# Optimization experiments

Hardware: AMD Instinct MI355X
Metric: run time of the kernel (lower is better)

## Reference

```python
import jax, jax.numpy as jnp
import numpy as np

NOT_EPSILON = 1.0
B, S, D = 1, 512, 256


def swishmax(x, axis):
    xexp = x * jnp.exp(x - jnp.max(x, axis=axis, keepdims=True))
    return xexp / (jnp.sum(jnp.abs(xexp), axis=axis, keepdims=True) + NOT_EPSILON)


def setup_inputs() -> dict:
    key = jax.random.key(0)
    ks = jax.random.split(key, 13)
    scale = 1.0 / np.sqrt(D)
    mk = lambda k: jax.random.uniform(k, (D, D), jnp.float32, -scale, scale)
    mb = lambda k: jax.random.uniform(k, (D,), jnp.float32, -scale, scale)
    return {
        "query_tokens": jax.random.normal(ks[0], (B, S, D), jnp.float32),
        "key_tokens": jax.random.normal(ks[1], (B, S, D), jnp.float32),
        "value_tokens": jax.random.normal(ks[2], (B, S, D), jnp.float32),
        "Wk": mk(ks[3]), "bk": mb(ks[4]),
        "Wq": mk(ks[5]), "bq": mb(ks[6]),
        "Wva": mk(ks[7]), "bva": mb(ks[8]),
        "Wl": mk(ks[9]), "bl": mb(ks[10]),
        "Wvo": mk(ks[11]), "bvo": mb(ks[12]),
    }


def reference(query_tokens, key_tokens, value_tokens,
              Wk, bk, Wq, bq, Wva, bva, Wl, bl, Wvo, bvo):
    # residual linear transforms of tokens
    k = key_tokens + key_tokens @ Wk + bk        # [B,S,D]
    q = query_tokens + query_tokens @ Wq + bq    # [B,S,D]
    # batchify: key -> [B,Sk,1,D], query -> [B,1,Sq,D]; outer-product scores
    attention_raw = k[:, :, None, :] * q[:, None, :, :]          # [B,Sk,Sq,D]
    attention_logits = attention_raw + attention_raw @ Wl + bl   # DxD linear on raw scores
    attention_scale = swishmax(attention_logits, axis=-2)        # normalize over query axis (dim -shape_dims)
    v = value_tokens + value_tokens @ Wva + bva  # [B,S,D]
    values_scaled = v[:, :, None, :] * attention_scale           # [B,Sk,Sq,D]
    value_sum = values_scaled.sum(axis=-3)                       # reduce key axis -> [B,Sq,D]
    value_out = value_sum + value_sum @ Wvo + bvo
    return value_out
```

## Files before the change

### kernel.cpp

```cpp
#include <hip/hip_runtime.h>
#include <math.h>

#define S_LEN 512
#define D_DIM 256
#define SLICE (S_LEN * D_DIM)

typedef _Float16 half8  __attribute__((ext_vector_type(8)));
typedef _Float16 half4v __attribute__((ext_vector_type(4)));
typedef float   floatx4 __attribute__((ext_vector_type(4)));

__global__ __launch_bounds__(256) void prep_wl(const float* __restrict__ Wl,
                                               _Float16* __restrict__ WlhT)
{
    const int d = blockIdx.x, e = threadIdx.x;
    float v = Wl[e * D_DIM + d] + (e == d ? 1.0f : 0.0f);
    WlhT[d * D_DIM + e] = (_Float16)v;
}

__global__ __launch_bounds__(256) void cvt_fp16(const float* __restrict__ kf,
                                                const float* __restrict__ qf,
                                                _Float16* __restrict__ kh,
                                                _Float16* __restrict__ qh)
{
    const int i = (blockIdx.x * 256 + threadIdx.x) * 4;
    float4 a = *(const float4*)(kf + i);
    float4 b = *(const float4*)(qf + i);
    half4v ah = { (_Float16)a.x, (_Float16)a.y, (_Float16)a.z, (_Float16)a.w };
    half4v bh = { (_Float16)b.x, (_Float16)b.y, (_Float16)b.z, (_Float16)b.w };
    *(half4v*)(kh + i) = ah;
    *(half4v*)(qh + i) = bh;
}

__global__ __launch_bounds__(256) void linres3(
    const float* __restrict__ xk, const float* __restrict__ Wk,
    const float* __restrict__ bk, float* __restrict__ yk,
    const float* __restrict__ xq, const float* __restrict__ Wq,
    const float* __restrict__ bq, float* __restrict__ yq,
    const float* __restrict__ xv, const float* __restrict__ Wv,
    const float* __restrict__ bv, float* __restrict__ yv)
{
    __shared__ float xs[4][D_DIM];
    const int r0 = blockIdx.x * 4;
    const int sel = blockIdx.y;
    const float* x = sel == 0 ? xk : (sel == 1 ? xq : xv);
    const float* W = sel == 0 ? Wk : (sel == 1 ? Wq : Wv);
    const float* b = sel == 0 ? bk : (sel == 1 ? bq : bv);
    float*       y = sel == 0 ? yk : (sel == 1 ? yq : yv);

    const int tid = threadIdx.x;
    #pragma unroll
    for (int t = 0; t < 4; ++t) xs[t][tid] = x[(r0 + t) * D_DIM + tid];
    __syncthreads();
    const float bv_ = b[tid];
    float acc[4];
    #pragma unroll
    for (int i = 0; i < 4; ++i) acc[i] = xs[i][tid] + bv_;
    #pragma unroll 4
    for (int e = 0; e < D_DIM; ++e) {
        const float w = W[e * D_DIM + tid];
        #pragma unroll
        for (int i = 0; i < 4; ++i) acc[i] += xs[i][e] * w;
    }
    #pragma unroll
    for (int i = 0; i < 4; ++i) y[(r0 + i) * D_DIM + tid] = acc[i];
}

__global__ __launch_bounds__(256) void linres_sum(
    const float* __restrict__ po, const float* __restrict__ W,
    const float* __restrict__ b, float* __restrict__ y)
{
    __shared__ float xs[4][D_DIM];
    const int tid = threadIdx.x;
    const int r0  = blockIdx.x * 4;
    #pragma unroll
    for (int t = 0; t < 4; ++t) {
        float s = 0.f;
        #pragma unroll
        for (int c = 0; c < 16; ++c)
            s += po[(size_t)c * SLICE + (r0 + t) * D_DIM + tid];
        xs[t][tid] = s;
    }
    __syncthreads();
    const float bv_ = b[tid];
    float acc[4];
    #pragma unroll
    for (int i = 0; i < 4; ++i) acc[i] = xs[i][tid] + bv_;
    #pragma unroll 4
    for (int e = 0; e < D_DIM; ++e) {
        const float w = W[e * D_DIM + tid];
        #pragma unroll
        for (int i = 0; i < 4; ++i) acc[i] += xs[i][e] * w;
    }
    #pragma unroll
    for (int i = 0; i < 4; ++i) y[(r0 + i) * D_DIM + tid] = acc[i];
}

__device__ __forceinline__ void stage_q(const _Float16* __restrict__ qh,
                                        _Float16* __restrict__ Afrag,
                                        int sq0, int tid)
{
    const int i   = tid & 63;
    const int qtr = tid >> 6;
    const int mt = i >> 4, l16 = i & 15;
    const half8* src = (const half8*)(qh + (size_t)(sq0 + i) * D_DIM + qtr * 64);
    #pragma unroll
    for (int u = 0; u < 8; ++u) {
        const int eb   = qtr * 8 + u;
        const int kk   = eb >> 2, quad = eb & 3;
        const int addr16 = (mt * 8 + kk) * 64 + quad * 16 + l16;
        *(half8*)(Afrag + addr16 * 8) = src[u];
    }
}

__device__ __forceinline__ void stage_q32(const _Float16* __restrict__ qh,
                                          _Float16* __restrict__ Afrag,
                                          int sq0, int tid)
{
    const int i   = tid & 31;
    const int oct = tid >> 5;
    const int mt = i >> 4, l16 = i & 15;
    const half8* src = (const half8*)(qh + (size_t)(sq0 + i) * D_DIM);
    #pragma unroll
    for (int u = 0; u < 4; ++u) {
        const int eb   = oct * 4 + u;
        const int kk   = eb >> 2, quad = eb & 3;
        const int addr16 = (mt * 8 + kk) * 64 + quad * 16 + l16;
        *(half8*)(Afrag + addr16 * 8) = src[eb];
    }
}

__global__ __launch_bounds__(256, 2) void stats_mfma(
    const _Float16* __restrict__ qh, const _Float16* __restrict__ kh,
    const _Float16* __restrict__ WlhT, const float* __restrict__ bl,
    float* __restrict__ pm, float* __restrict__ ps)
{
    __shared__ _Float16 Afrag[32 * 64 * 8];

    const int tid  = threadIdx.x;
    const int lane = tid & 63, wave = tid >> 6;
    const int quad = lane >> 4, l16 = lane & 15;
    const int sqt  = blockIdx.x, sq0 = sqt * 64;
    const int dw   = blockIdx.y * 128 + wave * 32;
    const int sk0  = blockIdx.z * 16;

    stage_q(qh, Afrag, sq0, tid);

    half8 wl[2][8];
    #pragma unroll
    for (int nt = 0; nt < 2; ++nt) {
        const int d = dw + nt * 16 + l16;
        #pragma unroll
        for (int kk = 0; kk < 8; ++kk)
            wl[nt][kk] = *(const half8*)(WlhT + (size_t)d * D_DIM + kk * 32 + quad * 8);
    }
    float bl_r[2];
    #pragma unroll
    for (int nt = 0; nt < 2; ++nt)
        bl_r[nt] = bl[dw + nt * 16 + l16];

    __syncthreads();

    #pragma unroll 1
    for (int s = 0; s < 16; ++s) {
        const int sk = sk0 + s;
        floatx4 acc[4][2];
        #pragma unroll
        for (int mt = 0; mt < 4; ++mt)
            #pragma unroll
            for (int nt = 0; nt < 2; ++nt)
                acc[mt][nt] = (floatx4){0.f, 0.f, 0.f, 0.f};

        #pragma unroll
        for (int kk = 0; kk < 8; ++kk) {
            const half8 k8 = *(const half8*)(kh + (size_t)sk * D_DIM + kk * 32 + quad * 8);
            half8 af[4], bf[2];
            #pragma unroll
            for (int mt = 0; mt < 4; ++mt)
                af[mt] = *(const half8*)(Afrag + ((mt * 8 + kk) * 64 + lane) * 8);
            #pragma unroll
            for (int nt = 0; nt < 2; ++nt)
                bf[nt] = wl[nt][kk] * k8;
            #pragma unroll
            for (int mt = 0; mt < 4; ++mt)
                #pragma unroll
                for (int nt = 0; nt < 2; ++nt)
                    acc[mt][nt] = __builtin_amdgcn_mfma_f32_16x16x32_f16(
                        af[mt], bf[nt], acc[mt][nt], 0, 0, 0);
        }

        #pragma unroll
        for (int nt = 0; nt < 2; ++nt) {
            float Lv[4][4];
            float tmax = -1e30f;
            #pragma unroll
            for (int mt = 0; mt < 4; ++mt)
                #pragma unroll
                for (int r = 0; r < 4; ++r) {
                    const float L = acc[mt][nt][r] + bl_r[nt];
                    Lv[mt][r] = L;
                    tmax = fmaxf(tmax, L);
                }
            float tsum = 0.f;
            #pragma unroll
            for (int mt = 0; mt < 4; ++mt)
                #pragma unroll
                for (int r = 0; r < 4; ++r)
                    tsum += fabsf(Lv[mt][r]) * __expf(Lv[mt][r] - tmax);

            float m = tmax, ss = tsum;
            #pragma unroll
            for (int mask = 16; mask <= 32; mask <<= 1) {
                float m2 = __shfl_xor(m, mask, 64);
                float s2 = __shfl_xor(ss, mask, 64);
                float M  = fmaxf(m, m2);
                ss = ss * __expf(m - M) + s2 * __expf(m2 - M);
                m = M;
            }
            if (quad == 0) {
                const int d = dw + nt * 16 + l16;
                pm[((size_t)sqt * S_LEN + sk) * D_DIM + d] = m;
                ps[((size_t)sqt * S_LEN + sk) * D_DIM + d] = ss;
            }
        }
    }
}

__global__ __launch_bounds__(256) void reduce_ms(
    const float* __restrict__ pm, const float* __restrict__ ps,
    float* __restrict__ mbuf, float* __restrict__ sbuf)
{
    const int idx = blockIdx.x * 256 + threadIdx.x;
    float m = pm[idx], ss = ps[idx];
    #pragma unroll
    for (int t = 1; t < 8; ++t) {
        const float m2 = pm[t * SLICE + idx];
        const float s2 = ps[t * SLICE + idx];
        const float M  = fmaxf(m, m2);
        ss = ss * __expf(m - M) + s2 * __expf(m2 - M);
        m = M;
    }
    mbuf[idx] = m;
    sbuf[idx] = ss;
}

__global__ __launch_bounds__(256, 2) void accum_mfma(
    const _Float16* __restrict__ qh, const _Float16* __restrict__ kh,
    const _Float16* __restrict__ WlhT, const float* __restrict__ bl,
    const float* __restrict__ mbuf, const float* __restrict__ sbuf,
    const float* __restrict__ vbuf, float* __restrict__ po)
{
    __shared__ _Float16 Afrag[16 * 64 * 8];

    const int tid  = threadIdx.x;
    const int lane = tid & 63, wave = tid >> 6;
    const int quad = lane >> 4, l16 = lane & 15;
    const int sq0  = blockIdx.x * 32;
    const int dw   = blockIdx.y * 128 + wave * 32;
    const int chunk = blockIdx.z;
    const int sk0  = chunk * 32;

    stage_q32(qh, Afrag, sq0, tid);

    half8 wl[2][8];
    #pragma unroll
    for (int nt = 0; nt < 2; ++nt) {
        const int d = dw + nt * 16 + l16;
        #pragma unroll
        for (int kk = 0; kk < 8; ++kk)
            wl[nt][kk] = *(const half8*)(WlhT + (size_t)d * D_DIM + kk * 32 + quad * 8);
    }
    float bl_r[2];
    #pragma unroll
    for (int nt = 0; nt < 2; ++nt)
        bl_r[nt] = bl[dw + nt * 16 + l16];

    floatx4 o[2][2];
    #pragma unroll
    for (int mt = 0; mt < 2; ++mt)
        #pragma unroll
        for (int nt = 0; nt < 2; ++nt)
            o[mt][nt] = (floatx4){0.f, 0.f, 0.f, 0.f};

    __syncthreads();

    #pragma unroll 1
    for (int s = 0; s < 32; ++s) {
        const int sk = sk0 + s;
        floatx4 acc[2][2];
        #pragma unroll
        for (int mt = 0; mt < 2; ++mt)
            #pragma unroll
            for (int nt = 0; nt < 2; ++nt)
                acc[mt][nt] = (floatx4){0.f, 0.f, 0.f, 0.f};

        #pragma unroll
        for (int kk = 0; kk < 8; ++kk) {
            const half8 k8 = *(const half8*)(kh + (size_t)sk * D_DIM + kk * 32 + quad * 8);
            half8 af[2], bf[2];
            #pragma unroll
            for (int mt = 0; mt < 2; ++mt)
                af[mt] = *(const half8*)(Afrag + ((mt * 8 + kk) * 64 + lane) * 8);
            #pragma unroll
            for (int nt = 0; nt < 2; ++nt)
                bf[nt] = wl[nt][kk] * k8;
            #pragma unroll
            for (int mt = 0; mt < 2; ++mt)
                #pragma unroll
                for (int nt = 0; nt < 2; ++nt)
                    acc[mt][nt] = __builtin_amdgcn_mfma_f32_16x16x32_f16(
                        af[mt], bf[nt], acc[mt][nt], 0, 0, 0);
        }

        #pragma unroll
        for (int nt = 0; nt < 2; ++nt) {
            const int d = dw + nt * 16 + l16;
            const float m_r = mbuf[(size_t)sk * D_DIM + d];
            const float inv = 1.0f / (sbuf[(size_t)sk * D_DIM + d] + 1.0f);
            const float vv  = vbuf[(size_t)sk * D_DIM + d];
            #pragma unroll
            for (int mt = 0; mt < 2; ++mt)
                #pragma unroll
                for (int r = 0; r < 4; ++r) {
                    const float L = acc[mt][nt][r] + bl_r[nt];
                    const float p = L * __expf(L - m_r) * inv;
                    o[mt][nt][r] += vv * p;
                }
        }
    }

    float* dst = po + (size_t)chunk * SLICE;
    #pragma unroll
    for (int mt = 0; mt < 2; ++mt)
        #pragma unroll
        for (int nt = 0; nt < 2; ++nt)
            #pragma unroll
            for (int r = 0; r < 4; ++r) {
                const int row = sq0 + mt * 16 + quad * 4 + r;
                const int col = dw + nt * 16 + l16;
                dst[(size_t)row * D_DIM + col] = o[mt][nt][r];
            }
}

extern "C" void kernel_launch(void* const* d_in, const int* in_sizes, int n_in,
                              void* d_out, int out_size, void* d_ws, size_t ws_size,
                              hipStream_t stream)
{
    const float* query = (const float*)d_in[0];
    const float* key   = (const float*)d_in[1];
    const float* value = (const float*)d_in[2];
    const float* Wk  = (const float*)d_in[3];
    const float* bk  = (const float*)d_in[4];
    const float* Wq  = (const float*)d_in[5];
    const float* bq  = (const float*)d_in[6];
    const float* Wva = (const float*)d_in[7];
    const float* bva = (const float*)d_in[8];
    const float* Wl  = (const float*)d_in[9];
    const float* bl  = (const float*)d_in[10];
    const float* Wvo = (const float*)d_in[11];
    const float* bvo = (const float*)d_in[12];

    const int MAT = SLICE;
    float* ws   = (float*)d_ws;
    float* kbuf = ws;
    float* qbuf = ws + MAT;
    float* vbuf = ws + 2 * MAT;
    float* mbuf = ws + 3 * MAT;
    float* sbuf = ws + 4 * MAT;
    _Float16* WlhT = (_Float16*)(ws + 6 * MAT);
    _Float16* kh   = (_Float16*)(ws + 6 * MAT + 32768);
    _Float16* qh   = kh + MAT;
    float* pm  = ws + 6 * MAT + 32768 + 2 * 65536;
    float* ps  = pm + 8 * MAT;
    float* po  = pm;
    float* out = (float*)d_out;

    prep_wl<<<256, 256, 0, stream>>>(Wl, WlhT);
    linres3<<<dim3(128, 3), 256, 0, stream>>>(key, Wk, bk, kbuf,
                                              query, Wq, bq, qbuf,
                                              value, Wva, bva, vbuf);
    cvt_fp16<<<128, 256, 0, stream>>>(kbuf, qbuf, kh, qh);

    stats_mfma<<<dim3(8, 2, 32), 256, 0, stream>>>(qh, kh, WlhT, bl, pm, ps);
    reduce_ms<<<512, 256, 0, stream>>>(pm, ps, mbuf, sbuf);
    accum_mfma<<<dim3(16, 2, 16), 256, 0, stream>>>(qh, kh, WlhT, bl,
                                                    mbuf, sbuf, vbuf, po);

    linres_sum<<<128, 256, 0, stream>>>(po, Wvo, bvo, out);
}
```

Before: 219.0 us.

## Fuse fp16 conversion into linres3 and shrink tiles to raise block counts

Removes the separate cvt_fp16 kernel by having linres3 write fp16 k and q directly. It halves rows per block in linres3 and linres_sum, halves the sk range per block in stats_mfma, and halves the query tile in accum_mfma while raising its launch-bounds occupancy target. Together these launch more blocks to fill the CUs and drop a kernel launch plus one round trip through memory. reduce_ms is also rewritten to load all partials first and do a two-pass max then sum. The smaller tiles reuse less data per block: each kernel reloads weights more often, and accum_mfma gets fewer MFMAs per k load.

```diff
diff --git a/kernel.cpp b/kernel.cpp
--- a/kernel.cpp
+++ b/kernel.cpp
@@ -17,63 +17,54 @@
     WlhT[d * D_DIM + e] = (_Float16)v;
 }
 
-__global__ __launch_bounds__(256) void cvt_fp16(const float* __restrict__ kf,
-                                                const float* __restrict__ qf,
-                                                _Float16* __restrict__ kh,
-                                                _Float16* __restrict__ qh)
-{
-    const int i = (blockIdx.x * 256 + threadIdx.x) * 4;
-    float4 a = *(const float4*)(kf + i);
-    float4 b = *(const float4*)(qf + i);
-    half4v ah = { (_Float16)a.x, (_Float16)a.y, (_Float16)a.z, (_Float16)a.w };
-    half4v bh = { (_Float16)b.x, (_Float16)b.y, (_Float16)b.z, (_Float16)b.w };
-    *(half4v*)(kh + i) = ah;
-    *(half4v*)(qh + i) = bh;
-}
-
 __global__ __launch_bounds__(256) void linres3(
     const float* __restrict__ xk, const float* __restrict__ Wk,
-    const float* __restrict__ bk, float* __restrict__ yk,
+    const float* __restrict__ bk, _Float16* __restrict__ yk16,
     const float* __restrict__ xq, const float* __restrict__ Wq,
-    const float* __restrict__ bq, float* __restrict__ yq,
+    const float* __restrict__ bq, _Float16* __restrict__ yq16,
     const float* __restrict__ xv, const float* __restrict__ Wv,
     const float* __restrict__ bv, float* __restrict__ yv)
 {
-    __shared__ float xs[4][D_DIM];
-    const int r0 = blockIdx.x * 4;
+    __shared__ float xs[2][D_DIM];
+    const int r0 = blockIdx.x * 2;
     const int sel = blockIdx.y;
     const float* x = sel == 0 ? xk : (sel == 1 ? xq : xv);
     const float* W = sel == 0 ? Wk : (sel == 1 ? Wq : Wv);
     const float* b = sel == 0 ? bk : (sel == 1 ? bq : bv);
-    float*       y = sel == 0 ? yk : (sel == 1 ? yq : yv);
 
     const int tid = threadIdx.x;
     #pragma unroll
-    for (int t = 0; t < 4; ++t) xs[t][tid] = x[(r0 + t) * D_DIM + tid];
+    for (int t = 0; t < 2; ++t) xs[t][tid] = x[(r0 + t) * D_DIM + tid];
     __syncthreads();
     const float bv_ = b[tid];
-    float acc[4];
-    #pragma unroll
-    for (int i = 0; i < 4; ++i) acc[i] = xs[i][tid] + bv_;
+    float acc[2];
+    #pragma unroll
+    for (int i = 0; i < 2; ++i) acc[i] = xs[i][tid] + bv_;
     #pragma unroll 4
     for (int e = 0; e < D_DIM; ++e) {
         const float w = W[e * D_DIM + tid];
         #pragma unroll
-        for (int i = 0; i < 4; ++i) acc[i] += xs[i][e] * w;
-    }
-    #pragma unroll
-    for (int i = 0; i < 4; ++i) y[(r0 + i) * D_DIM + tid] = acc[i];
+        for (int i = 0; i < 2; ++i) acc[i] += xs[i][e] * w;
+    }
+    if (sel == 2) {
+        #pragma unroll
+        for (int i = 0; i < 2; ++i) yv[(r0 + i) * D_DIM + tid] = acc[i];
+    } else {
+        _Float16* y16 = sel == 0 ? yk16 : yq16;
+        #pragma unroll
+        for (int i = 0; i < 2; ++i) y16[(r0 + i) * D_DIM + tid] = (_Float16)acc[i];
+    }
 }
 
 __global__ __launch_bounds__(256) void linres_sum(
     const float* __restrict__ po, const float* __restrict__ W,
     const float* __restrict__ b, float* __restrict__ y)
 {
-    __shared__ float xs[4][D_DIM];
+    __shared__ float xs[2][D_DIM];
     const int tid = threadIdx.x;
-    const int r0  = blockIdx.x * 4;
-    #pragma unroll
-    for (int t = 0; t < 4; ++t) {
+    const int r0  = blockIdx.x * 2;
+    #pragma unroll
+    for (int t = 0; t < 2; ++t) {
         float s = 0.f;
         #pragma unroll
         for (int c = 0; c < 16; ++c)
@@ -82,17 +73,17 @@
     }
     __syncthreads();
     const float bv_ = b[tid];
-    float acc[4];
-    #pragma unroll
-    for (int i = 0; i < 4; ++i) acc[i] = xs[i][tid] + bv_;
+    float acc[2];
+    #pragma unroll
+    for (int i = 0; i < 2; ++i) acc[i] = xs[i][tid] + bv_;
     #pragma unroll 4
     for (int e = 0; e < D_DIM; ++e) {
         const float w = W[e * D_DIM + tid];
         #pragma unroll
-        for (int i = 0; i < 4; ++i) acc[i] += xs[i][e] * w;
-    }
-    #pragma unroll
-    for (int i = 0; i < 4; ++i) y[(r0 + i) * D_DIM + tid] = acc[i];
+        for (int i = 0; i < 2; ++i) acc[i] += xs[i][e] * w;
+    }
+    #pragma unroll
+    for (int i = 0; i < 2; ++i) y[(r0 + i) * D_DIM + tid] = acc[i];
 }
 
 __device__ __forceinline__ void stage_q(const _Float16* __restrict__ qh,
@@ -112,19 +103,18 @@
     }
 }
 
-__device__ __forceinline__ void stage_q32(const _Float16* __restrict__ qh,
+__device__ __forceinline__ void stage_q16(const _Float16* __restrict__ qh,
                                           _Float16* __restrict__ Afrag,
                                           int sq0, int tid)
 {
-    const int i   = tid & 31;
-    const int oct = tid >> 5;
-    const int mt = i >> 4, l16 = i & 15;
+    const int i  = tid & 15;
+    const int sx = tid >> 4;
     const half8* src = (const half8*)(qh + (size_t)(sq0 + i) * D_DIM);
     #pragma unroll
-    for (int u = 0; u < 4; ++u) {
-        const int eb   = oct * 4 + u;
+    for (int u = 0; u < 2; ++u) {
+        const int eb   = sx * 2 + u;
         const int kk   = eb >> 2, quad = eb & 3;
-        const int addr16 = (mt * 8 + kk) * 64 + quad * 16 + l16;
+        const int addr16 = kk * 64 + quad * 16 + i;
         *(half8*)(Afrag + addr16 * 8) = src[eb];
     }
 }
@@ -141,7 +131,7 @@
     const int quad = lane >> 4, l16 = lane & 15;
     const int sqt  = blockIdx.x, sq0 = sqt * 64;
     const int dw   = blockIdx.y * 128 + wave * 32;
-    const int sk0  = blockIdx.z * 16;
+    const int sk0  = blockIdx.z * 8;
 
     stage_q(qh, Afrag, sq0, tid);
 
@@ -161,7 +151,7 @@
     __syncthreads();
 
     #pragma unroll 1
-    for (int s = 0; s < 16; ++s) {
+    for (int s = 0; s < 8; ++s) {
         const int sk = sk0 + s;
         floatx4 acc[4][2];
         #pragma unroll
@@ -230,36 +220,39 @@
     float* __restrict__ mbuf, float* __restrict__ sbuf)
 {
     const int idx = blockIdx.x * 256 + threadIdx.x;
-    float m = pm[idx], ss = ps[idx];
-    #pragma unroll
-    for (int t = 1; t < 8; ++t) {
-        const float m2 = pm[t * SLICE + idx];
-        const float s2 = ps[t * SLICE + idx];
-        const float M  = fmaxf(m, m2);
-        ss = ss * __expf(m - M) + s2 * __expf(m2 - M);
-        m = M;
-    }
-    mbuf[idx] = m;
+    float mv[8], sv[8];
+    #pragma unroll
+    for (int t = 0; t < 8; ++t) {
+        mv[t] = pm[(size_t)t * SLICE + idx];
+        sv[t] = ps[(size_t)t * SLICE + idx];
+    }
+    float M = mv[0];
+    #pragma unroll
+    for (int t = 1; t < 8; ++t) M = fmaxf(M, mv[t]);
+    float ss = 0.f;
+    #pragma unroll
+    for (int t = 0; t < 8; ++t) ss += sv[t] * __expf(mv[t] - M);
+    mbuf[idx] = M;
     sbuf[idx] = ss;
 }
 
-__global__ __launch_bounds__(256, 2) void accum_mfma(
+__global__ __launch_bounds__(256, 4) void accum_mfma(
     const _Float16* __restrict__ qh, const _Float16* __restrict__ kh,
     const _Float16* __restrict__ WlhT, const float* __restrict__ bl,
     const float* __restrict__ mbuf, const float* __restrict__ sbuf,
     const float* __restrict__ vbuf, float* __restrict__ po)
 {
-    __shared__ _Float16 Afrag[16 * 64 * 8];
+    __shared__ _Float16 Afrag[8 * 64 * 8];
 
     const int tid  = threadIdx.x;
     const int lane = tid & 63, wave = tid >> 6;
     const int quad = lane >> 4, l16 = lane & 15;
-    const int sq0  = blockIdx.x * 32;
+    const int sq0  = blockIdx.x * 16;
     const int dw   = blockIdx.y * 128 + wave * 32;
     const int chunk = blockIdx.z;
     const int sk0  = chunk * 32;
 
-    stage_q32(qh, Afrag, sq0, tid);
+    stage_q16(qh, Afrag, sq0, tid);
 
     half8 wl[2][8];
     #pragma unroll
@@ -274,41 +267,33 @@
     for (int nt = 0; nt < 2; ++nt)
         bl_r[nt] = bl[dw + nt * 16 + l16];
 
-    floatx4 o[2][2];
-    #pragma unroll
-    for (int mt = 0; mt < 2; ++mt)
-        #pragma unroll
-        for (int nt = 0; nt < 2; ++nt)
-            o[mt][nt] = (floatx4){0.f, 0.f, 0.f, 0.f};
+    floatx4 o[2];
+    #pragma unroll
+    for (int nt = 0; nt < 2; ++nt)
+        o[nt] = (floatx4){0.f, 0.f, 0.f, 0.f};
 
     __syncthreads();
 
     #pragma unroll 1
     for (int s = 0; s < 32; ++s) {
         const int sk = sk0 + s;
-        floatx4 acc[2][2];
-        #pragma unroll
-        for (int mt = 0; mt < 2; ++mt)
-            #pragma unroll
-            for (int nt = 0; nt < 2; ++nt)
-                acc[mt][nt] = (floatx4){0.f, 0.f, 0.f, 0.f};
+        floatx4 acc[2];
+        #pragma unroll
+        for (int nt = 0; nt < 2; ++nt)
+            acc[nt] = (floatx4){0.f, 0.f, 0.f, 0.f};
 
         #pragma unroll
         for (int kk = 0; kk < 8; ++kk) {
             const half8 k8 = *(const half8*)(kh + (size_t)sk * D_DIM + kk * 32 + quad * 8);
-            half8 af[2], bf[2];
-            #pragma unroll
-            for (int mt = 0; mt < 2; ++mt)
-                af[mt] = *(const half8*)(Afrag + ((mt * 8 + kk) * 64 + lane) * 8);
+            const half8 af = *(const half8*)(Afrag + (kk * 64 + lane) * 8);
+            half8 bf[2];
             #pragma unroll
             for (int nt = 0; nt < 2; ++nt)
                 bf[nt] = wl[nt][kk] * k8;
             #pragma unroll
-            for (int mt = 0; mt < 2; ++mt)
-                #pragma unroll
-                for (int nt = 0; nt < 2; ++nt)
-                    acc[mt][nt] = __builtin_amdgcn_mfma_f32_16x16x32_f16(
-                        af[mt], bf[nt], acc[mt][nt], 0, 0, 0);
+            for (int nt = 0; nt < 2; ++nt)
+                acc[nt] = __builtin_amdgcn_mfma_f32_16x16x32_f16(
+                    af, bf[nt], acc[nt], 0, 0, 0);
         }
 
         #pragma unroll
@@ -318,27 +303,23 @@
             const float inv = 1.0f / (sbuf[(size_t)sk * D_DIM + d] + 1.0f);
             const float vv  = vbuf[(size_t)sk * D_DIM + d];
             #pragma unroll
-            for (int mt = 0; mt < 2; ++mt)
-                #pragma unroll
-                for (int r = 0; r < 4; ++r) {
-                    const float L = acc[mt][nt][r] + bl_r[nt];
-                    const float p = L * __expf(L - m_r) * inv;
-                    o[mt][nt][r] += vv * p;
-                }
+            for (int r = 0; r < 4; ++r) {
+                const float L = acc[nt][r] + bl_r[nt];
+                const float p = L * __expf(L - m_r) * inv;
+                o[nt][r] += vv * p;
+            }
         }
     }
 
     float* dst = po + (size_t)chunk * SLICE;
     #pragma unroll
-    for (int mt = 0; mt < 2; ++mt)
-        #pragma unroll
-        for (int nt = 0; nt < 2; ++nt)
-            #pragma unroll
-            for (int r = 0; r < 4; ++r) {
-                const int row = sq0 + mt * 16 + quad * 4 + r;
-                const int col = dw + nt * 16 + l16;
-                dst[(size_t)row * D_DIM + col] = o[mt][nt][r];
-            }
+    for (int nt = 0; nt < 2; ++nt)
+        #pragma unroll
+        for (int r = 0; r < 4; ++r) {
+            const int row = sq0 + quad * 4 + r;
+            const int col = dw + nt * 16 + l16;
+            dst[(size_t)row * D_DIM + col] = o[nt][r];
+        }
 }
 
 extern "C" void kernel_launch(void* const* d_in, const int* in_sizes, int n_in,
@@ -361,8 +342,6 @@
 
     const int MAT = SLICE;
     float* ws   = (float*)d_ws;
-    float* kbuf = ws;
-    float* qbuf = ws + MAT;
     float* vbuf = ws + 2 * MAT;
     float* mbuf = ws + 3 * MAT;
     float* sbuf = ws + 4 * MAT;
@@ -375,15 +354,14 @@
     float* out = (float*)d_out;
 
     prep_wl<<<256, 256, 0, stream>>>(Wl, WlhT);
-    linres3<<<dim3(128, 3), 256, 0, stream>>>(key, Wk, bk, kbuf,
-                                              query, Wq, bq, qbuf,
+    linres3<<<dim3(256, 3), 256, 0, stream>>>(key, Wk, bk, kh,
+                                              query, Wq, bq, qh,
                                               value, Wva, bva, vbuf);
-    cvt_fp16<<<128, 256, 0, stream>>>(kbuf, qbuf, kh, qh);
-
-    stats_mfma<<<dim3(8, 2, 32), 256, 0, stream>>>(qh, kh, WlhT, bl, pm, ps);
+
+    stats_mfma<<<dim3(8, 2, 64), 256, 0, stream>>>(qh, kh, WlhT, bl, pm, ps);
     reduce_ms<<<512, 256, 0, stream>>>(pm, ps, mbuf, sbuf);
-    accum_mfma<<<dim3(16, 2, 16), 256, 0, stream>>>(qh, kh, WlhT, bl,
+    accum_mfma<<<dim3(32, 2, 16), 256, 0, stream>>>(qh, kh, WlhT, bl,
                                                     mbuf, sbuf, vbuf, po);
 
-    linres_sum<<<128, 256, 0, stream>>>(po, Wvo, bvo, out);
-}
+    linres_sum<<<256, 256, 0, stream>>>(po, Wvo, bvo, out);
+}
```

After: 300.1 us. 1.37x slower.
